# Kernel optimization log

Hardware: AMD Instinct MI355X
Metric: run time of the kernel (lower is better)

Reference implementation:

```python
import jax, jax.numpy as jnp
import numpy as np

D = 512          # sequence_dim
H = 8            # num_heads
DA = 64          # attn_dim per head
DV = 64          # linear_dim per head
NB = 4           # num_blocks
N = 1024         # max_seq_length + max_output_len + 1
B = 4
EPS = 1e-6


def setup_inputs() -> dict:
    key = jax.random.key(0)
    ks = jax.random.split(key, 8)
    sequence = jax.random.normal(ks[0], (B, N, D), dtype=jnp.float32)
    sequence_length = jax.random.randint(ks[1], (B,), 1, 1014)
    pos_embed = jax.random.normal(ks[2], (N, D), dtype=jnp.float32)  # nn.Embedding ~ N(0,1)
    w_uvqk = jax.random.normal(ks[3], (NB, D, 2 * H * DV + 2 * H * DA), dtype=jnp.float32) * 0.02
    w_o = jax.random.normal(ks[4], (NB, H * DV, D), dtype=jnp.float32) * 0.02
    b_o = jnp.zeros((NB, D), dtype=jnp.float32)
    ln1_g = jnp.ones((NB, D), dtype=jnp.float32)
    ln1_b = jnp.zeros((NB, D), dtype=jnp.float32)
    ln2_g = jnp.ones((NB, H * DV), dtype=jnp.float32)
    ln2_b = jnp.zeros((NB, H * DV), dtype=jnp.float32)
    pos_w = jax.random.normal(ks[5], (NB, 2 * N - 1), dtype=jnp.float32) * 0.02
    return {
        'sequence': sequence, 'sequence_length': sequence_length,
        'pos_embed': pos_embed, 'ln1_g': ln1_g, 'ln1_b': ln1_b,
        'w_uvqk': w_uvqk, 'ln2_g': ln2_g, 'ln2_b': ln2_b,
        'w_o': w_o, 'b_o': b_o, 'pos_w': pos_w,
    }


def _layer_norm(x, g, b):
    mu = jnp.mean(x, axis=-1, keepdims=True)
    var = jnp.mean(jnp.square(x - mu), axis=-1, keepdims=True)
    return (x - mu) * jax.lax.rsqrt(var + EPS) * g + b


def reference(sequence, sequence_length, pos_embed, ln1_g, ln1_b, w_uvqk,
              ln2_g, ln2_b, w_o, b_o, pos_w):
    # positional embedding + scale (inference: dropout = identity)
    x = sequence * jnp.asarray(np.sqrt(D), sequence.dtype) + pos_embed[None, :, :]
    # length mask (dense-padded equivalent of the jagged representation)
    mask = (jnp.arange(N)[None, :] < sequence_length[:, None]).astype(sequence.dtype)[..., None]
    x = x * mask
    # invalid_attn_mask = 1 - triu(ones, diag=1): causal incl. diagonal
    causal = jnp.tril(jnp.ones((N, N), sequence.dtype))
    # rel_pos_bias[i, j] = pos_w[j - i + N - 1]
    idx = jnp.arange(N)
    rel = idx[None, :] - idx[:, None] + (N - 1)  # (N, N) in [0, 2N-2]
    for l in range(NB):
        nx = _layer_norm(x, ln1_g[l], ln1_b[l])
        uvqk = jax.nn.silu(nx @ w_uvqk[l])  # (B, N, 2*H*DV + 2*H*DA)
        u, v, q, k = jnp.split(uvqk, [H * DV, 2 * H * DV, 2 * H * DV + H * DA], axis=-1)
        qh = q.reshape(x.shape[0], N, H, DA)
        kh = k.reshape(x.shape[0], N, H, DA)
        vh = v.reshape(x.shape[0], N, H, DV)
        qk = jnp.einsum('bnhd,bmhd->bhnm', qh, kh) + pos_w[l][rel][None, None]
        attn = jax.nn.silu(qk) * (causal / N)  # (B, H, N, N)
        av = jnp.einsum('bhnm,bmhd->bnhd', attn, vh).reshape(x.shape[0], N, H * DV)
        o_in = _layer_norm(av, ln2_g[l], ln2_b[l]) * u
        x = (x + o_in @ w_o[l] + b_o[l]) * mask  # mask = dense<->jagged roundtrip
    # output_embeddings[..., :D] then L2-normalize with clamped norm
    norm = jnp.linalg.norm(x, axis=-1, keepdims=True)
    return x / jnp.clip(norm, 1e-6, None)
```

## Files before the change

### kernel.cpp

```cpp
#include <hip/hip_runtime.h>
#include <math.h>
#include <stdint.h>

#define NN 1024
#define ROWS 4096
#define NBL 4

typedef _Float16 h8 __attribute__((ext_vector_type(8)));
typedef _Float16 h4 __attribute__((ext_vector_type(4)));
typedef float f4 __attribute__((ext_vector_type(4)));

__device__ __forceinline__ float fast_silu(float x) {
    float e = __builtin_amdgcn_exp2f(-1.4426950408889634f * x);
    return x * __builtin_amdgcn_rcpf(1.0f + e);
}

__device__ __forceinline__ void gl16(const void* gp, void* lp) {
    __builtin_amdgcn_global_load_lds(
        (const __attribute__((address_space(1))) uint32_t*)gp,
        (__attribute__((address_space(3))) uint32_t*)lp, 16, 0, 0);
}

__device__ __forceinline__ float wred(float s) {
    #pragma unroll
    for (int off = 1; off < 64; off <<= 1) s += __shfl_xor(s, off);
    return s;
}

__global__ __launch_bounds__(256) void k_transpose16(const float* __restrict__ wuvqk,
                                                     _Float16* __restrict__ wuT,
                                                     const float* __restrict__ wo,
                                                     _Float16* __restrict__ woT) {
    __shared__ _Float16 T[64][66];
    int z = blockIdx.z;
    const float* s; _Float16* d; int N;
    if (z < 4) { N = 2048; s = wuvqk + (size_t)z * 512 * 2048; d = wuT + (size_t)z * 2048 * 512; }
    else {
        if (blockIdx.x >= 8) return;
        N = 512; s = wo + (size_t)(z - 4) * 512 * 512; d = woT + (size_t)(z - 4) * 512 * 512;
    }
    int n0 = blockIdx.x << 6, k0 = blockIdx.y << 6;
    int tx = threadIdx.x & 63, ty = threadIdx.x >> 6;
    #pragma unroll
    for (int q = 0; q < 16; ++q)
        T[(q << 2) + ty][tx] = (_Float16)s[(size_t)(k0 + (q << 2) + ty) * N + n0 + tx];
    __syncthreads();
    #pragma unroll
    for (int q = 0; q < 16; ++q)
        d[(size_t)(n0 + (q << 2) + ty) * 512 + k0 + tx] = T[tx][(q << 2) + ty];
}

template<int MODE>
__global__ __launch_bounds__(256) void k_lnw(const float* __restrict__ X,
                                             const float* __restrict__ X2,
                                             const float* __restrict__ X3,
                                             const float* __restrict__ seq,
                                             const float* __restrict__ pos,
                                             const int* __restrict__ slen,
                                             const float* __restrict__ g,
                                             const float* __restrict__ bt,
                                             _Float16* __restrict__ O,
                                             const _Float16* __restrict__ U,
                                             float* __restrict__ Xw) {
    int tid = threadIdx.x;
    int w = tid >> 6, lane = tid & 63;
    int c = lane << 3;
    #pragma unroll
    for (int rr = 0; rr < 2; ++rr) {
        int row = (blockIdx.x << 3) + (w << 1) + rr;
        float v[8];
        if (MODE == 1) {
            int b = row >> 10, n = row & (NN - 1);
            float m = (n < slen[b]) ? 1.0f : 0.0f;
            const float4* sp = (const float4*)&seq[(size_t)row * 512 + c];
            const float4* pp = (const float4*)&pos[(size_t)n * 512 + c];
            const float SD = 22.627416997969522f;
            float4 s0 = sp[0], s1 = sp[1], p0 = pp[0], p1 = pp[1];
            v[0]=(s0.x*SD+p0.x)*m; v[1]=(s0.y*SD+p0.y)*m; v[2]=(s0.z*SD+p0.z)*m; v[3]=(s0.w*SD+p0.w)*m;
            v[4]=(s1.x*SD+p1.x)*m; v[5]=(s1.y*SD+p1.y)*m; v[6]=(s1.z*SD+p1.z)*m; v[7]=(s1.w*SD+p1.w)*m;
            float4 o0, o1;
            o0.x=v[0]; o0.y=v[1]; o0.z=v[2]; o0.w=v[3];
            o1.x=v[4]; o1.y=v[5]; o1.z=v[6]; o1.w=v[7];
            float4* xp = (float4*)&Xw[(size_t)row * 512 + c];
            xp[0] = o0; xp[1] = o1;
        } else {
            const float4* xp = (const float4*)&X[(size_t)row * 512 + c];
            float4 a = xp[0], b4 = xp[1];
            v[0]=a.x; v[1]=a.y; v[2]=a.z; v[3]=a.w; v[4]=b4.x; v[5]=b4.y; v[6]=b4.z; v[7]=b4.w;
            if (MODE == 2) {
                int nn = row & (NN - 1);
                if (nn >= 384) {
                    const float4* qp = (const float4*)&X2[(size_t)row * 512 + c];
                    float4 t0 = qp[0], t1 = qp[1];
                    v[0]+=t0.x; v[1]+=t0.y; v[2]+=t0.z; v[3]+=t0.w;
                    v[4]+=t1.x; v[5]+=t1.y; v[6]+=t1.z; v[7]+=t1.w;
                }
                if (nn >= 768) {
                    const float4* qp = (const float4*)&X3[(size_t)row * 512 + c];
                    float4 t0 = qp[0], t1 = qp[1];
                    v[0]+=t0.x; v[1]+=t0.y; v[2]+=t0.z; v[3]+=t0.w;
                    v[4]+=t1.x; v[5]+=t1.y; v[6]+=t1.z; v[7]+=t1.w;
                }
            }
        }
        float s = v[0]+v[1]+v[2]+v[3]+v[4]+v[5]+v[6]+v[7];
        s = wred(s);
        float mu = s * (1.0f / 512.0f);
        float ss = 0.0f;
        #pragma unroll
        for (int i = 0; i < 8; ++i) { float d = v[i] - mu; ss += d * d; }
        ss = wred(ss);
        float rs = rsqrtf(ss * (1.0f / 512.0f) + 1e-6f);

        const float4* gp = (const float4*)&g[c];
        const float4* bp = (const float4*)&bt[c];
        float4 g0 = gp[0], g1 = gp[1], b0 = bp[0], b1 = bp[1];
        float gg[8] = {g0.x,g0.y,g0.z,g0.w,g1.x,g1.y,g1.z,g1.w};
        float bb[8] = {b0.x,b0.y,b0.z,b0.w,b1.x,b1.y,b1.z,b1.w};
        float o[8];
        #pragma unroll
        for (int i = 0; i < 8; ++i) o[i] = (v[i] - mu) * rs * gg[i] + bb[i];
        if (MODE == 2) {
            h8 uu = *(const h8*)&U[(size_t)row * 2048 + c];
            #pragma unroll
            for (int i = 0; i < 8; ++i) o[i] *= (float)uu[i];
        }
        h8 oh;
        #pragma unroll
        for (int i = 0; i < 8; ++i) oh[i] = (_Float16)o[i];
        *(h8*)&O[(size_t)row * 512 + c] = oh;
    }
}

__global__ __launch_bounds__(256) void k_normw(float* __restrict__ X) {
    int tid = threadIdx.x;
    int w = tid >> 6, lane = tid & 63;
    int c = lane << 3;
    #pragma unroll
    for (int rr = 0; rr < 2; ++rr) {
        int row = (blockIdx.x << 3) + (w << 1) + rr;
        float4* xp = (float4*)&X[(size_t)row * 512 + c];
        float4 a = xp[0], b4 = xp[1];
        float ss = a.x*a.x + a.y*a.y + a.z*a.z + a.w*a.w +
                   b4.x*b4.x + b4.y*b4.y + b4.z*b4.z + b4.w*b4.w;
        ss = wred(ss);
        float sc = 1.0f / fmaxf(sqrtf(ss), 1e-6f);
        a.x*=sc; a.y*=sc; a.z*=sc; a.w*=sc; b4.x*=sc; b4.y*=sc; b4.z*=sc; b4.w*=sc;
        xp[0] = a; xp[1] = b4;
    }
}

template<int EPI, int BM, int BN, int WAVES, int WGR, int WGC>
__global__ __launch_bounds__(WAVES * 64) void k_gemm(const _Float16* __restrict__ A,
                                                     const _Float16* __restrict__ Bm,
                                                     _Float16* __restrict__ Cu,
                                                     _Float16* __restrict__ vT,
                                                     const float* __restrict__ bo,
                                                     const int* __restrict__ slen,
                                                     float* __restrict__ Xio) {
    constexpr int WR = BM / WGR / 16;
    constexpr int WC = BN / WGC / 16;
    constexpr int QA = BM * 8 / (WAVES * 64);
    constexpr int QB = BN * 8 / (WAVES * 64);
    __shared__ _Float16 smem[2 * 64 * (BM + BN)];
    _Float16* AsB = smem;
    _Float16* BsB = smem + 2 * BM * 64;
    int tid = threadIdx.x;
    int w = tid >> 6, lane = tid & 63;
    int t = lane & 15, gq = lane >> 4;
    int flat = blockIdx.y * gridDim.x + blockIdx.x;
    int cpx = (gridDim.x * gridDim.y) >> 3;
    int f2 = (flat & 7) * cpx + (flat >> 3);
    int bx = f2 % gridDim.x, by = f2 / gridDim.x;
    int row0 = by * BM, col0 = bx * BN;
    int wr = (w / WGC) * (BM / WGR), wc = (w % WGC) * (BN / WGC);

    f4 zero4 = {0.0f, 0.0f, 0.0f, 0.0f};
    f4 acc[WR][WC];
    #pragma unroll
    for (int i = 0; i < WR; ++i)
        #pragma unroll
        for (int j = 0; j < WC; ++j) acc[i][j] = zero4;

    auto stage = [&](int buf, int k0) {
        _Float16* As = AsB + buf * BM * 64;
        _Float16* Bs = BsB + buf * BN * 64;
        #pragma unroll
        for (int q = 0; q < QA; ++q) {
            int s = (q * WAVES + w) * 64 + lane;
            int r = s >> 3, cs = (s & 7) ^ (r & 7);
            gl16(A + (size_t)(row0 + r) * 512 + k0 + (cs << 3),
                 (char*)As + (size_t)(q * WAVES + w) * 1024);
        }
        #pragma unroll
        for (int q = 0; q < QB; ++q) {
            int s = (q * WAVES + w) * 64 + lane;
            int r = s >> 3, cs = (s & 7) ^ (r & 7);
            gl16(Bm + (size_t)(col0 + r) * 512 + k0 + (cs << 3),
                 (char*)Bs + (size_t)(q * WAVES + w) * 1024);
        }
    };

    stage(0, 0);
    int cur = 0;
    for (int k0 = 0; k0 < 512; k0 += 64) {
        __syncthreads();
        if (k0 + 64 < 512) stage(cur ^ 1, k0 + 64);
        const char* As = (const char*)(AsB + cur * BM * 64);
        const char* Bs = (const char*)(BsB + cur * BN * 64);
        h8 af[WR][2], bf[WC][2];
        #pragma unroll
        for (int i = 0; i < WR; ++i) {
            int rl = wr + (i << 4) + t;
            #pragma unroll
            for (int ks = 0; ks < 2; ++ks)
                af[i][ks] = *(const h8*)(As + rl * 128 + (((gq + (ks << 2)) ^ (rl & 7)) << 4));
        }
        #pragma unroll
        for (int j = 0; j < WC; ++j) {
            int nl = wc + (j << 4) + t;
            #pragma unroll
            for (int ks = 0; ks < 2; ++ks)
                bf[j][ks] = *(const h8*)(Bs + nl * 128 + (((gq + (ks << 2)) ^ (nl & 7)) << 4));
        }
        #pragma unroll
        for (int i = 0; i < WR; ++i)
            #pragma unroll
            for (int j = 0; j < WC; ++j) {
                acc[i][j] = __builtin_amdgcn_mfma_f32_16x16x32_f16(af[i][0], bf[j][0], acc[i][j], 0, 0, 0);
                acc[i][j] = __builtin_amdgcn_mfma_f32_16x16x32_f16(af[i][1], bf[j][1], acc[i][j], 0, 0, 0);
            }
        cur ^= 1;
    }

    if (EPI == 0) {
        _Float16* E = smem;
        bool vblk = (col0 >= 512 && col0 < 1024);
        __syncthreads();
        if (vblk) {
            #pragma unroll
            for (int i = 0; i < WR; ++i)
                #pragma unroll
                for (int j = 0; j < WC; ++j) {
                    int cl = wc + (j << 4) + t;
                    int rl = wr + (i << 4) + (gq << 2);
                    h4 pk;
                    #pragma unroll
                    for (int rr = 0; rr < 4; ++rr) pk[rr] = (_Float16)fast_silu(acc[i][j][rr]);
                    *(h4*)&E[cl * 136 + rl] = pk;
                }
        } else {
            #pragma unroll
            for (int i = 0; i < WR; ++i)
                #pragma unroll
                for (int j = 0; j < WC; ++j) {
                    int cl = wc + (j << 4) + t;
                    int rl = wr + (i << 4) + (gq << 2);
                    #pragma unroll
                    for (int rr = 0; rr < 4; ++rr)
                        E[(rl + rr) * 136 + cl] = (_Float16)fast_silu(acc[i][j][rr]);
                }
        }
        __syncthreads();
        constexpr int ITERS = 128 * 16 / (WAVES * 64);
        if (vblk) {
            int b = row0 >> 10;
            int n0l = row0 & 1023;
            #pragma unroll
            for (int it = 0; it < ITERS; ++it) {
                int dl = it * (WAVES * 4) + (tid >> 4);
                int cc = tid & 15;
                h8 vv = *(const h8*)&E[dl * 136 + (cc << 3)];
                int hh = (col0 + dl - 512) >> 6, dd = (col0 + dl - 512) & 63;
                *(h8*)&vT[((size_t)((b << 3) + hh) * 64 + dd) * 1024 + n0l + (cc << 3)] = vv;
            }
        } else {
            #pragma unroll
            for (int it = 0; it < ITERS; ++it) {
                int rl = it * (WAVES * 4) + (tid >> 4);
                int cc = tid & 15;
                h8 vv = *(const h8*)&E[rl * 136 + (cc << 3)];
                *(h8*)&Cu[(size_t)(row0 + rl) * 2048 + col0 + (cc << 3)] = vv;
            }
        }
    } else {
        #pragma unroll
        for (int i = 0; i < WR; ++i) {
            #pragma unroll
            for (int j = 0; j < WC; ++j) {
                int colf = col0 + wc + (j << 4) + t;
                int rowb = row0 + wr + (i << 4) + (gq << 2);
                int b = rowb >> 10;
                #pragma unroll
                for (int rr = 0; rr < 4; ++rr) {
                    int row = rowb + rr;
                    float m = ((row & 1023) < slen[b]) ? 1.0f : 0.0f;
                    size_t ix = (size_t)row * 512 + colf;
                    Xio[ix] = (Xio[ix] + acc[i][j][rr] + bo[colf]) * m;
                }
            }
        }
    }
}

__global__ __launch_bounds__(256) void k_attn(const _Float16* __restrict__ uvqk,
                                              const _Float16* __restrict__ vT,
                                              const float* __restrict__ posw,
                                              float* __restrict__ av0,
                                              float* __restrict__ av1,
                                              float* __restrict__ av2) {
    __shared__ _Float16 Ks[2][64 * 64];
    __shared__ _Float16 Vs[64 * 64];
    __shared__ _Float16 Ps[64 * 72];
    __shared__ float pws[2][128];
    int tid = threadIdx.x;
    int w = tid >> 6, lane = tid & 63;
    int t = lane & 15, gq = lane >> 4;
    int flat = blockIdx.x + 30 * (blockIdx.y + 8 * blockIdx.z);
    int f2 = (flat & 7) * 120 + (flat >> 3);
    int u = f2 % 30, h = (f2 / 30) & 7, b = f2 / 240;

    int nt, mlo, mhi;
    float* avout;
    if (u < 6) { nt = u; mlo = 0; mhi = nt; avout = av0; }
    else if (u < 18) {
        int p = u - 6; nt = 6 + (p >> 1);
        int c0 = (nt + 2) >> 1;
        if (p & 1) { mlo = c0; mhi = nt; avout = av1; }
        else       { mlo = 0;  mhi = c0 - 1; avout = av0; }
    } else {
        int p = u - 18; int third = p / 3; nt = 12 + third; int q3 = p - 3 * third;
        int c = nt + 1, c1 = (c + 2) / 3, c2 = (2 * c + 2) / 3;
        if (q3 == 0)      { mlo = 0;  mhi = c1 - 1; avout = av0; }
        else if (q3 == 1) { mlo = c1; mhi = c2 - 1; avout = av1; }
        else              { mlo = c2; mhi = nt;     avout = av2; }
    }
    int n0 = nt << 6;

    const _Float16* qbase = uvqk + (size_t)b * NN * 2048 + 1024 + h * 64;
    const _Float16* kbase = uvqk + (size_t)b * NN * 2048 + 1536 + h * 64;
    const _Float16* vbase = vT + (size_t)((b << 3) + h) * 64 * 1024;

    #pragma unroll
    for (int q = 0; q < 2; ++q) {
        int s = (((w << 1) + q) << 6) + lane;
        int r = s >> 3, cs = (s & 7) ^ (r & 7);
        gl16(qbase + (size_t)(n0 + r) * 2048 + (cs << 3),
             (char*)&Ks[1][0] + (size_t)(((w << 1) + q) << 6) * 16);
        gl16(kbase + (size_t)((mlo << 6) + r) * 2048 + (cs << 3),
             (char*)&Ks[0][0] + (size_t)(((w << 1) + q) << 6) * 16);
    }
    if (tid < 128) pws[0][tid] = posw[(mlo << 6) - n0 + tid + 960];
    __syncthreads();

    h8 aq[2];
    {
        int rl = (w << 4) + t;
        #pragma unroll
        for (int ks = 0; ks < 2; ++ks)
            aq[ks] = *(const h8*)((const char*)&Ks[1][0] + rl * 128 +
                                  (((gq + (ks << 2)) ^ (rl & 7)) << 4));
    }
    asm volatile("s_waitcnt lgkmcnt(0)" ::: "memory");
    __builtin_amdgcn_sched_barrier(0);
    __syncthreads();

    f4 zero4 = {0.0f, 0.0f, 0.0f, 0.0f};
    f4 avacc[4];
    #pragma unroll
    for (int j = 0; j < 4; ++j) avacc[j] = zero4;

    int cur = 0;
    for (int mt = mlo; mt <= mhi; ++mt) {
        int m0 = mt << 6;
        #pragma unroll
        for (int q = 0; q < 2; ++q) {
            int s = (((w << 1) + q) << 6) + lane;
            int r = s >> 3, cs = (s & 7) ^ (r & 7);
            gl16(vbase + (size_t)r * 1024 + m0 + (cs << 3),
                 (char*)&Vs[0] + (size_t)(((w << 1) + q) << 6) * 16);
        }
        int mt2 = (mt < mhi) ? mt + 1 : mt;
        #pragma unroll
        for (int q = 0; q < 2; ++q) {
            int s = (((w << 1) + q) << 6) + lane;
            int r = s >> 3, cs = (s & 7) ^ (r & 7);
            gl16(kbase + (size_t)((mt2 << 6) + r) * 2048 + (cs << 3),
                 (char*)&Ks[cur ^ 1][0] + (size_t)(((w << 1) + q) << 6) * 16);
        }
        if (tid < 128) pws[cur ^ 1][tid] = posw[(mt2 << 6) - n0 + tid + 960];

        f4 sacc[4];
        __builtin_amdgcn_s_setprio(1);
        #pragma unroll
        for (int i = 0; i < 4; ++i) {
            f4 binit;
            #pragma unroll
            for (int rr = 0; rr < 4; ++rr)
                binit[rr] = pws[cur][63 + (i << 4) + (gq << 2) + rr - ((w << 4) + t)];
            int ml = (i << 4) + t;
            h8 ak0 = *(const h8*)((const char*)&Ks[cur][0] + ml * 128 + (((gq + 0) ^ (ml & 7)) << 4));
            h8 ak1 = *(const h8*)((const char*)&Ks[cur][0] + ml * 128 + (((gq + 4) ^ (ml & 7)) << 4));
            sacc[i] = __builtin_amdgcn_mfma_f32_16x16x32_f16(ak0, aq[0], binit, 0, 0, 0);
            sacc[i] = __builtin_amdgcn_mfma_f32_16x16x32_f16(ak1, aq[1], sacc[i], 0, 0, 0);
        }
        __builtin_amdgcn_s_setprio(0);
        int nabs = n0 + (w << 4) + t;
        #pragma unroll
        for (int i = 0; i < 4; ++i) {
            int mb = m0 + (i << 4) + (gq << 2);
            h4 pk;
            #pragma unroll
            for (int rr = 0; rr < 4; ++rr) {
                float p = (mb + rr <= nabs) ? fast_silu(sacc[i][rr]) : 0.0f;
                pk[rr] = (_Float16)p;
            }
            *(h4*)((char*)Ps + ((w << 4) + t) * 144 + (i << 5) + (gq << 3)) = pk;
        }
        asm volatile("s_waitcnt lgkmcnt(0)" ::: "memory");
        asm volatile("s_waitcnt vmcnt(2)" ::: "memory");
        __builtin_amdgcn_s_barrier();
        __builtin_amdgcn_s_setprio(1);
        #pragma unroll
        for (int ks = 0; ks < 2; ++ks) {
            h8 pa = *(const h8*)((const char*)Ps + ((w << 4) + t) * 144 + (ks << 6) + (gq << 4));
            #pragma unroll
            for (int jt = 0; jt < 4; ++jt) {
                int dl = (jt << 4) + t;
                h8 bv = *(const h8*)((const char*)&Vs[0] + dl * 128 +
                                     (((gq + (ks << 2)) ^ (dl & 7)) << 4));
                avacc[jt] = __builtin_amdgcn_mfma_f32_16x16x32_f16(pa, bv, avacc[jt], 0, 0, 0);
            }
        }
        __builtin_amdgcn_s_setprio(0);
        __syncthreads();
        cur ^= 1;
    }

    #pragma unroll
    for (int jt = 0; jt < 4; ++jt) {
        #pragma unroll
        for (int rr = 0; rr < 4; ++rr) {
            int n = n0 + (w << 4) + (gq << 2) + rr;
            int d = (jt << 4) + t;
            avout[(size_t)(b * NN + n) * 512 + h * 64 + d] = avacc[jt][rr] * (1.0f / 1024.0f);
        }
    }
}

extern "C" void kernel_launch(void* const* d_in, const int* in_sizes, int n_in,
                              void* d_out, int out_size, void* d_ws, size_t ws_size,
                              hipStream_t stream) {
    const float* seq   = (const float*)d_in[0];
    const int*   slen  = (const int*)d_in[1];
    const float* pos   = (const float*)d_in[2];
    const float* ln1g  = (const float*)d_in[3];
    const float* ln1b  = (const float*)d_in[4];
    const float* wuvqk = (const float*)d_in[5];
    const float* ln2g  = (const float*)d_in[6];
    const float* ln2b  = (const float*)d_in[7];
    const float* wo    = (const float*)d_in[8];
    const float* bo    = (const float*)d_in[9];
    const float* posw  = (const float*)d_in[10];

    float* x = (float*)d_out;
    char* W = (char*)d_ws;
    _Float16* nx16   = (_Float16*)(W);
    _Float16* oin16  = (_Float16*)(W + (4u << 20));
    _Float16* uvqk16 = (_Float16*)(W + (8u << 20));
    _Float16* vT16   = (_Float16*)(W + (24u << 20));
    float*    av0    = (float*)   (W + (28u << 20));
    float*    av1    = (float*)   (W + (36u << 20));
    float*    av2    = (float*)   (W + (44u << 20));
    _Float16* wuT16  = (_Float16*)(W + (52u << 20));
    _Float16* woT16  = (_Float16*)(W + (60u << 20));

    k_transpose16<<<dim3(32, 8, 8), 256, 0, stream>>>(wuvqk, wuT16, wo, woT16);
    for (int l = 0; l < NBL; ++l) {
        if (l == 0)
            k_lnw<1><<<512, 256, 0, stream>>>(nullptr, nullptr, nullptr, seq, pos, slen,
                                              ln1g, ln1b, nx16, nullptr, x);
        else
            k_lnw<0><<<512, 256, 0, stream>>>(x, nullptr, nullptr, nullptr, nullptr, nullptr,
                                              ln1g + l * 512, ln1b + l * 512, nx16, nullptr, nullptr);
        k_gemm<0, 128, 128, 8, 2, 4><<<dim3(16, 32), 512, 0, stream>>>(
            nx16, wuT16 + (size_t)l * 2048 * 512, uvqk16, vT16, nullptr, nullptr, nullptr);
        k_attn<<<dim3(30, 8, NBL), 256, 0, stream>>>(uvqk16, vT16, posw + l * (2 * NN - 1),
                                                     av0, av1, av2);
        k_lnw<2><<<512, 256, 0, stream>>>(av0, av1, av2, nullptr, nullptr, nullptr,
                                          ln2g + l * 512, ln2b + l * 512, oin16, uvqk16, nullptr);
        k_gemm<1, 64, 32, 4, 2, 2><<<dim3(16, 64), 256, 0, stream>>>(
            oin16, woT16 + (size_t)l * 512 * 512, nullptr, nullptr, bo + l * 512, slen, x);
    }
    k_normw<<<512, 256, 0, stream>>>(x);
}
```

Baseline: 208.7 us.

## Fuse all layer stages into one cooperative persistent megakernel with grid syncs

Replaces the sequence of about 22 kernel launches with a single cooperative kernel of 512 blocks that loops over transpose, layernorm, GEMM, attention and norm stages, separated by grid-wide syncs. Attention work units are taken from an atomic work queue in a fixed heavy-first order, so the causal load imbalance is spread across blocks. The uvqk GEMM now uses 4 waves instead of 8 per tile. The aim is to remove launch overhead and inter-kernel gaps, at the cost of grid.sync latency, a 64 KB static shared allocation that limits occupancy to 2 blocks per CU, and less efficient GEMM tiling. The old multi-launch path is kept as a fallback when cooperative launch is unavailable.

```diff
diff --git a/kernel.cpp b/kernel.cpp
--- a/kernel.cpp
+++ b/kernel.cpp
@@ -1,6 +1,9 @@
 #include <hip/hip_runtime.h>
+#include <hip/hip_cooperative_groups.h>
 #include <math.h>
 #include <stdint.h>
+
+namespace cg = cooperative_groups;
 
 #define NN 1024
 #define ROWS 4096
@@ -27,20 +30,25 @@
     return s;
 }
 
-__global__ __launch_bounds__(256) void k_transpose16(const float* __restrict__ wuvqk,
-                                                     _Float16* __restrict__ wuT,
-                                                     const float* __restrict__ wo,
-                                                     _Float16* __restrict__ woT) {
-    __shared__ _Float16 T[64][66];
-    int z = blockIdx.z;
-    const float* s; _Float16* d; int N;
-    if (z < 4) { N = 2048; s = wuvqk + (size_t)z * 512 * 2048; d = wuT + (size_t)z * 2048 * 512; }
-    else {
-        if (blockIdx.x >= 8) return;
-        N = 512; s = wo + (size_t)(z - 4) * 512 * 512; d = woT + (size_t)(z - 4) * 512 * 512;
-    }
-    int n0 = blockIdx.x << 6, k0 = blockIdx.y << 6;
-    int tx = threadIdx.x & 63, ty = threadIdx.x >> 6;
+__constant__ int c_order[30] = {5,14,16,17,27, 4,10,12,13,15,18,21,22,24,25,26,28,29,
+                                3,6,8,9,11,19,20,23, 2,7, 1, 0};
+
+__device__ void transpose_unit(int u, char* smem,
+                               const float* __restrict__ wuvqk, _Float16* __restrict__ wuT,
+                               const float* __restrict__ wo, _Float16* __restrict__ woT) {
+    _Float16 (*T)[66] = (_Float16 (*)[66])smem;
+    const float* s; _Float16* d; int N, n0, k0;
+    if (u < 1024) {
+        int z = u >> 8, t = u & 255;
+        N = 2048; s = wuvqk + (size_t)z * 512 * 2048; d = wuT + (size_t)z * 2048 * 512;
+        n0 = (t & 31) << 6; k0 = (t >> 5) << 6;
+    } else {
+        int r2 = u - 1024; int z = r2 >> 6, t = r2 & 63;
+        N = 512; s = wo + (size_t)z * 512 * 512; d = woT + (size_t)z * 512 * 512;
+        n0 = (t & 7) << 6; k0 = (t >> 3) << 6;
+    }
+    int tid = threadIdx.x, tx = tid & 63, ty = tid >> 6;
+    __syncthreads();
     #pragma unroll
     for (int q = 0; q < 16; ++q)
         T[(q << 2) + ty][tx] = (_Float16)s[(size_t)(k0 + (q << 2) + ty) * N + n0 + tx];
@@ -51,23 +59,19 @@
 }
 
 template<int MODE>
-__global__ __launch_bounds__(256) void k_lnw(const float* __restrict__ X,
-                                             const float* __restrict__ X2,
-                                             const float* __restrict__ X3,
-                                             const float* __restrict__ seq,
-                                             const float* __restrict__ pos,
-                                             const int* __restrict__ slen,
-                                             const float* __restrict__ g,
-                                             const float* __restrict__ bt,
-                                             _Float16* __restrict__ O,
-                                             const _Float16* __restrict__ U,
-                                             float* __restrict__ Xw) {
+__device__ void ln_unit(int vb,
+                        const float* __restrict__ X, const float* __restrict__ X2,
+                        const float* __restrict__ X3, const float* __restrict__ seq,
+                        const float* __restrict__ pos, const int* __restrict__ slen,
+                        const float* __restrict__ g, const float* __restrict__ bt,
+                        _Float16* __restrict__ O, const _Float16* __restrict__ U,
+                        float* __restrict__ Xw) {
     int tid = threadIdx.x;
     int w = tid >> 6, lane = tid & 63;
     int c = lane << 3;
     #pragma unroll
     for (int rr = 0; rr < 2; ++rr) {
-        int row = (blockIdx.x << 3) + (w << 1) + rr;
+        int row = (vb << 3) + (w << 1) + rr;
         float v[8];
         if (MODE == 1) {
             int b = row >> 10, n = row & (NN - 1);
@@ -132,13 +136,13 @@
     }
 }
 
-__global__ __launch_bounds__(256) void k_normw(float* __restrict__ X) {
+__device__ void norm_unit(int vb, float* __restrict__ X) {
     int tid = threadIdx.x;
     int w = tid >> 6, lane = tid & 63;
     int c = lane << 3;
     #pragma unroll
     for (int rr = 0; rr < 2; ++rr) {
-        int row = (blockIdx.x << 3) + (w << 1) + rr;
+        int row = (vb << 3) + (w << 1) + rr;
         float4* xp = (float4*)&X[(size_t)row * 512 + c];
         float4 a = xp[0], b4 = xp[1];
         float ss = a.x*a.x + a.y*a.y + a.z*a.z + a.w*a.w +
@@ -151,29 +155,27 @@
 }
 
 template<int EPI, int BM, int BN, int WAVES, int WGR, int WGC>
-__global__ __launch_bounds__(WAVES * 64) void k_gemm(const _Float16* __restrict__ A,
-                                                     const _Float16* __restrict__ Bm,
-                                                     _Float16* __restrict__ Cu,
-                                                     _Float16* __restrict__ vT,
-                                                     const float* __restrict__ bo,
-                                                     const int* __restrict__ slen,
-                                                     float* __restrict__ Xio) {
+__device__ void gemm_unit(int unit, int nbx, int nunits, char* smemc,
+                          const _Float16* __restrict__ A, const _Float16* __restrict__ Bm,
+                          _Float16* __restrict__ Cu, _Float16* __restrict__ vT,
+                          const float* __restrict__ bo, const int* __restrict__ slen,
+                          float* __restrict__ Xio) {
     constexpr int WR = BM / WGR / 16;
     constexpr int WC = BN / WGC / 16;
     constexpr int QA = BM * 8 / (WAVES * 64);
     constexpr int QB = BN * 8 / (WAVES * 64);
-    __shared__ _Float16 smem[2 * 64 * (BM + BN)];
-    _Float16* AsB = smem;
-    _Float16* BsB = smem + 2 * BM * 64;
+    _Float16* AsB = (_Float16*)smemc;
+    _Float16* BsB = (_Float16*)smemc + 2 * BM * 64;
     int tid = threadIdx.x;
     int w = tid >> 6, lane = tid & 63;
     int t = lane & 15, gq = lane >> 4;
-    int flat = blockIdx.y * gridDim.x + blockIdx.x;
-    int cpx = (gridDim.x * gridDim.y) >> 3;
-    int f2 = (flat & 7) * cpx + (flat >> 3);
-    int bx = f2 % gridDim.x, by = f2 / gridDim.x;
+    int cpx = nunits >> 3;
+    int f2 = (unit & 7) * cpx + (unit >> 3);
+    int bx = f2 % nbx, by = f2 / nbx;
     int row0 = by * BM, col0 = bx * BN;
     int wr = (w / WGC) * (BM / WGR), wc = (w % WGC) * (BN / WGC);
+
+    __syncthreads();
 
     f4 zero4 = {0.0f, 0.0f, 0.0f, 0.0f};
     f4 acc[WR][WC];
@@ -234,7 +236,7 @@
     }
 
     if (EPI == 0) {
-        _Float16* E = smem;
+        _Float16* E = (_Float16*)smemc;
         bool vblk = (col0 >= 512 && col0 < 1024);
         __syncthreads();
         if (vblk) {
@@ -303,25 +305,20 @@
     }
 }
 
-__global__ __launch_bounds__(256) void k_attn(const _Float16* __restrict__ uvqk,
-                                              const _Float16* __restrict__ vT,
-                                              const float* __restrict__ posw,
-                                              float* __restrict__ av0,
-                                              float* __restrict__ av1,
-                                              float* __restrict__ av2) {
-    __shared__ _Float16 Ks[2][64 * 64];
-    __shared__ _Float16 Vs[64 * 64];
-    __shared__ _Float16 Ps[64 * 72];
-    __shared__ float pws[2][128];
+__device__ void attn_unit(int b, int h, int u, char* smem,
+                          const _Float16* __restrict__ uvqk, const _Float16* __restrict__ vTg,
+                          const float* __restrict__ pw,
+                          float* __restrict__ av0, float* __restrict__ av1,
+                          float* __restrict__ av2) {
     int tid = threadIdx.x;
     int w = tid >> 6, lane = tid & 63;
     int t = lane & 15, gq = lane >> 4;
-    int flat = blockIdx.x + 30 * (blockIdx.y + 8 * blockIdx.z);
-    int f2 = (flat & 7) * 120 + (flat >> 3);
-    int u = f2 % 30, h = (f2 / 30) & 7, b = f2 / 240;
-
-    int nt, mlo, mhi;
-    float* avout;
+    char* KsBase = smem;
+    char* VsBase = smem + 16384;
+    char* Ps     = smem + 24576;
+    float* pws   = (float*)(smem + 33792);
+
+    int nt, mlo, mhi; float* avout;
     if (u < 6) { nt = u; mlo = 0; mhi = nt; avout = av0; }
     else if (u < 18) {
         int p = u - 6; nt = 6 + (p >> 1);
@@ -339,18 +336,16 @@
 
     const _Float16* qbase = uvqk + (size_t)b * NN * 2048 + 1024 + h * 64;
     const _Float16* kbase = uvqk + (size_t)b * NN * 2048 + 1536 + h * 64;
-    const _Float16* vbase = vT + (size_t)((b << 3) + h) * 64 * 1024;
+    const _Float16* vbase = vTg + (size_t)((b << 3) + h) * 64 * 1024;
 
     #pragma unroll
     for (int q = 0; q < 2; ++q) {
         int s = (((w << 1) + q) << 6) + lane;
         int r = s >> 3, cs = (s & 7) ^ (r & 7);
-        gl16(qbase + (size_t)(n0 + r) * 2048 + (cs << 3),
-             (char*)&Ks[1][0] + (size_t)(((w << 1) + q) << 6) * 16);
-        gl16(kbase + (size_t)((mlo << 6) + r) * 2048 + (cs << 3),
-             (char*)&Ks[0][0] + (size_t)(((w << 1) + q) << 6) * 16);
-    }
-    if (tid < 128) pws[0][tid] = posw[(mlo << 6) - n0 + tid + 960];
+        gl16(qbase + (size_t)(n0 + r) * 2048 + (cs << 3), KsBase + 8192 + (((w << 1) + q) << 10));
+        gl16(kbase + (size_t)((mlo << 6) + r) * 2048 + (cs << 3), KsBase + (((w << 1) + q) << 10));
+    }
+    if (tid < 128) pws[tid] = pw[(mlo << 6) - n0 + tid + 960];
     __syncthreads();
 
     h8 aq[2];
@@ -358,8 +353,7 @@
         int rl = (w << 4) + t;
         #pragma unroll
         for (int ks = 0; ks < 2; ++ks)
-            aq[ks] = *(const h8*)((const char*)&Ks[1][0] + rl * 128 +
-                                  (((gq + (ks << 2)) ^ (rl & 7)) << 4));
+            aq[ks] = *(const h8*)(KsBase + 8192 + rl * 128 + (((gq + (ks << 2)) ^ (rl & 7)) << 4));
     }
     asm volatile("s_waitcnt lgkmcnt(0)" ::: "memory");
     __builtin_amdgcn_sched_barrier(0);
@@ -377,8 +371,7 @@
         for (int q = 0; q < 2; ++q) {
             int s = (((w << 1) + q) << 6) + lane;
             int r = s >> 3, cs = (s & 7) ^ (r & 7);
-            gl16(vbase + (size_t)r * 1024 + m0 + (cs << 3),
-                 (char*)&Vs[0] + (size_t)(((w << 1) + q) << 6) * 16);
+            gl16(vbase + (size_t)r * 1024 + m0 + (cs << 3), VsBase + (((w << 1) + q) << 10));
         }
         int mt2 = (mt < mhi) ? mt + 1 : mt;
         #pragma unroll
@@ -386,10 +379,11 @@
             int s = (((w << 1) + q) << 6) + lane;
             int r = s >> 3, cs = (s & 7) ^ (r & 7);
             gl16(kbase + (size_t)((mt2 << 6) + r) * 2048 + (cs << 3),
-                 (char*)&Ks[cur ^ 1][0] + (size_t)(((w << 1) + q) << 6) * 16);
-        }
-        if (tid < 128) pws[cur ^ 1][tid] = posw[(mt2 << 6) - n0 + tid + 960];
-
+                 KsBase + ((cur ^ 1) << 13) + (((w << 1) + q) << 10));
+        }
+        if (tid < 128) pws[((cur ^ 1) << 7) + tid] = pw[(mt2 << 6) - n0 + tid + 960];
+
+        const char* Kc = KsBase + (cur << 13);
         f4 sacc[4];
         __builtin_amdgcn_s_setprio(1);
         #pragma unroll
@@ -397,10 +391,10 @@
             f4 binit;
             #pragma unroll
             for (int rr = 0; rr < 4; ++rr)
-                binit[rr] = pws[cur][63 + (i << 4) + (gq << 2) + rr - ((w << 4) + t)];
+                binit[rr] = pws[(cur << 7) + 63 + (i << 4) + (gq << 2) + rr - ((w << 4) + t)];
             int ml = (i << 4) + t;
-            h8 ak0 = *(const h8*)((const char*)&Ks[cur][0] + ml * 128 + (((gq + 0) ^ (ml & 7)) << 4));
-            h8 ak1 = *(const h8*)((const char*)&Ks[cur][0] + ml * 128 + (((gq + 4) ^ (ml & 7)) << 4));
+            h8 ak0 = *(const h8*)(Kc + ml * 128 + (((gq + 0) ^ (ml & 7)) << 4));
+            h8 ak1 = *(const h8*)(Kc + ml * 128 + (((gq + 4) ^ (ml & 7)) << 4));
             sacc[i] = __builtin_amdgcn_mfma_f32_16x16x32_f16(ak0, aq[0], binit, 0, 0, 0);
             sacc[i] = __builtin_amdgcn_mfma_f32_16x16x32_f16(ak1, aq[1], sacc[i], 0, 0, 0);
         }
@@ -415,7 +409,7 @@
                 float p = (mb + rr <= nabs) ? fast_silu(sacc[i][rr]) : 0.0f;
                 pk[rr] = (_Float16)p;
             }
-            *(h4*)((char*)Ps + ((w << 4) + t) * 144 + (i << 5) + (gq << 3)) = pk;
+            *(h4*)(Ps + ((w << 4) + t) * 144 + (i << 5) + (gq << 3)) = pk;
         }
         asm volatile("s_waitcnt lgkmcnt(0)" ::: "memory");
         asm volatile("s_waitcnt vmcnt(2)" ::: "memory");
@@ -423,12 +417,11 @@
         __builtin_amdgcn_s_setprio(1);
         #pragma unroll
         for (int ks = 0; ks < 2; ++ks) {
-            h8 pa = *(const h8*)((const char*)Ps + ((w << 4) + t) * 144 + (ks << 6) + (gq << 4));
+            h8 pa = *(const h8*)(Ps + ((w << 4) + t) * 144 + (ks << 6) + (gq << 4));
             #pragma unroll
             for (int jt = 0; jt < 4; ++jt) {
                 int dl = (jt << 4) + t;
-                h8 bv = *(const h8*)((const char*)&Vs[0] + dl * 128 +
-                                     (((gq + (ks << 2)) ^ (dl & 7)) << 4));
+                h8 bv = *(const h8*)(VsBase + dl * 128 + (((gq + (ks << 2)) ^ (dl & 7)) << 4));
                 avacc[jt] = __builtin_amdgcn_mfma_f32_16x16x32_f16(pa, bv, avacc[jt], 0, 0, 0);
             }
         }
@@ -448,49 +441,163 @@
     }
 }
 
+__global__ __launch_bounds__(256) void k_transpose16(const float* wuvqk, _Float16* wuT,
+                                                     const float* wo, _Float16* woT) {
+    __shared__ __align__(16) char smem[8448];
+    transpose_unit(blockIdx.x, smem, wuvqk, wuT, wo, woT);
+}
+
+template<int MODE>
+__global__ __launch_bounds__(256) void k_lnw(const float* X, const float* X2, const float* X3,
+                                             const float* seq, const float* pos, const int* slen,
+                                             const float* g, const float* bt,
+                                             _Float16* O, const _Float16* U, float* Xw) {
+    ln_unit<MODE>(blockIdx.x, X, X2, X3, seq, pos, slen, g, bt, O, U, Xw);
+}
+
+__global__ __launch_bounds__(256) void k_normw(float* X) { norm_unit(blockIdx.x, X); }
+
+template<int EPI, int BM, int BN, int WAVES, int WGR, int WGC>
+__global__ __launch_bounds__(WAVES * 64) void k_gemm(const _Float16* A, const _Float16* Bm,
+                                                     _Float16* Cu, _Float16* vT,
+                                                     const float* bo, const int* slen, float* Xio) {
+    __shared__ __align__(16) char smem[(BM + BN) * 256];
+    gemm_unit<EPI, BM, BN, WAVES, WGR, WGC>(blockIdx.y * gridDim.x + blockIdx.x, gridDim.x,
+                                            gridDim.x * gridDim.y, smem, A, Bm, Cu, vT, bo, slen, Xio);
+}
+
+__global__ __launch_bounds__(256) void k_attn(const _Float16* uvqk, const _Float16* vT,
+                                              const float* posw, float* av0, float* av1, float* av2) {
+    __shared__ __align__(16) char smem[34816];
+    int flat = blockIdx.x + 30 * (blockIdx.y + 8 * blockIdx.z);
+    int f2 = (flat & 7) * 120 + (flat >> 3);
+    int u = f2 % 30, h = (f2 / 30) & 7, b = f2 / 240;
+    attn_unit(b, h, u, smem, uvqk, vT, posw, av0, av1, av2);
+}
+
+struct MegaArgs {
+    const float *seq, *pos, *ln1g, *ln1b, *ln2g, *ln2b, *wuvqk, *wo, *bo, *posw;
+    const int* slen;
+    float *x, *av0, *av1, *av2;
+    _Float16 *nx, *oin, *uvqk, *vT, *wuT, *woT;
+    unsigned int* ctr;
+};
+
+__global__ __launch_bounds__(256, 2) void k_mega(MegaArgs P) {
+    cg::grid_group grid = cg::this_grid();
+    __shared__ __align__(16) char smem[65536];
+    int tid = threadIdx.x, bid = blockIdx.x, G = gridDim.x;
+
+    if (bid == 0 && tid < 4) atomicExch(&P.ctr[tid], 0u);
+    for (int u = bid; u < 1280; u += G)
+        transpose_unit(u, smem, P.wuvqk, P.wuT, P.wo, P.woT);
+    for (int vb = bid; vb < 512; vb += G)
+        ln_unit<1>(vb, nullptr, nullptr, nullptr, P.seq, P.pos, P.slen, P.ln1g, P.ln1b,
+                   P.nx, nullptr, P.x);
+    grid.sync();
+
+    for (int l = 0; l < NBL; ++l) {
+        if (l > 0) {
+            for (int vb = bid; vb < 512; vb += G)
+                ln_unit<0>(vb, P.x, nullptr, nullptr, nullptr, nullptr, nullptr,
+                           P.ln1g + l * 512, P.ln1b + l * 512, P.nx, nullptr, nullptr);
+            grid.sync();
+        }
+        for (int u = bid; u < 512; u += G)
+            gemm_unit<0, 128, 128, 4, 2, 2>(u, 16, 512, smem, P.nx,
+                                            P.wuT + (size_t)l * 2048 * 512,
+                                            P.uvqk, P.vT, nullptr, nullptr, nullptr);
+        grid.sync();
+        {
+            volatile int* sm_u = (volatile int*)(smem + 35840);
+            const float* pw = P.posw + l * 2047;
+            for (;;) {
+                __syncthreads();
+                if (tid == 0) *sm_u = (int)atomicAdd(&P.ctr[l], 1u);
+                __syncthreads();
+                int p = *sm_u;
+                if (p >= 960) break;
+                int bh = p & 31;
+                attn_unit(bh >> 3, bh & 7, c_order[p >> 5], smem, P.uvqk, P.vT, pw,
+                          P.av0, P.av1, P.av2);
+            }
+        }
+        grid.sync();
+        for (int vb = bid; vb < 512; vb += G)
+            ln_unit<2>(vb, P.av0, P.av1, P.av2, nullptr, nullptr, nullptr,
+                       P.ln2g + l * 512, P.ln2b + l * 512, P.oin, P.uvqk, nullptr);
+        grid.sync();
+        for (int u = bid; u < 1024; u += G)
+            gemm_unit<1, 64, 32, 4, 2, 2>(u, 16, 1024, smem, P.oin,
+                                          P.woT + (size_t)l * 512 * 512,
+                                          nullptr, nullptr, P.bo + l * 512, P.slen, P.x);
+        grid.sync();
+    }
+    for (int vb = bid; vb < 512; vb += G)
+        norm_unit(vb, P.x);
+}
+
 extern "C" void kernel_launch(void* const* d_in, const int* in_sizes, int n_in,
                               void* d_out, int out_size, void* d_ws, size_t ws_size,
                               hipStream_t stream) {
-    const float* seq   = (const float*)d_in[0];
-    const int*   slen  = (const int*)d_in[1];
-    const float* pos   = (const float*)d_in[2];
-    const float* ln1g  = (const float*)d_in[3];
-    const float* ln1b  = (const float*)d_in[4];
-    const float* wuvqk = (const float*)d_in[5];
-    const float* ln2g  = (const float*)d_in[6];
-    const float* ln2b  = (const float*)d_in[7];
-    const float* wo    = (const float*)d_in[8];
-    const float* bo    = (const float*)d_in[9];
-    const float* posw  = (const float*)d_in[10];
-
-    float* x = (float*)d_out;
     char* W = (char*)d_ws;
-    _Float16* nx16   = (_Float16*)(W);
-    _Float16* oin16  = (_Float16*)(W + (4u << 20));
-    _Float16* uvqk16 = (_Float16*)(W + (8u << 20));
-    _Float16* vT16   = (_Float16*)(W + (24u << 20));
-    float*    av0    = (float*)   (W + (28u << 20));
-    float*    av1    = (float*)   (W + (36u << 20));
-    float*    av2    = (float*)   (W + (44u << 20));
-    _Float16* wuT16  = (_Float16*)(W + (52u << 20));
-    _Float16* woT16  = (_Float16*)(W + (60u << 20));
-
-    k_transpose16<<<dim3(32, 8, 8), 256, 0, stream>>>(wuvqk, wuT16, wo, woT16);
-    for (int l = 0; l < NBL; ++l) {
-        if (l == 0)
-            k_lnw<1><<<512, 256, 0, stream>>>(nullptr, nullptr, nullptr, seq, pos, slen,
-                                              ln1g, ln1b, nx16, nullptr, x);
-        else
-            k_lnw<0><<<512, 256, 0, stream>>>(x, nullptr, nullptr, nullptr, nullptr, nullptr,
-                                              ln1g + l * 512, ln1b + l * 512, nx16, nullptr, nullptr);
-        k_gemm<0, 128, 128, 8, 2, 4><<<dim3(16, 32), 512, 0, stream>>>(
-            nx16, wuT16 + (size_t)l * 2048 * 512, uvqk16, vT16, nullptr, nullptr, nullptr);
-        k_attn<<<dim3(30, 8, NBL), 256, 0, stream>>>(uvqk16, vT16, posw + l * (2 * NN - 1),
-                                                     av0, av1, av2);
-        k_lnw<2><<<512, 256, 0, stream>>>(av0, av1, av2, nullptr, nullptr, nullptr,
-                                          ln2g + l * 512, ln2b + l * 512, oin16, uvqk16, nullptr);
-        k_gemm<1, 64, 32, 4, 2, 2><<<dim3(16, 64), 256, 0, stream>>>(
-            oin16, woT16 + (size_t)l * 512 * 512, nullptr, nullptr, bo + l * 512, slen, x);
-    }
-    k_normw<<<512, 256, 0, stream>>>(x);
-}
+    MegaArgs P;
+    P.seq   = (const float*)d_in[0];
+    P.slen  = (const int*)d_in[1];
+    P.pos   = (const float*)d_in[2];
+    P.ln1g  = (const float*)d_in[3];
+    P.ln1b  = (const float*)d_in[4];
+    P.wuvqk = (const float*)d_in[5];
+    P.ln2g  = (const float*)d_in[6];
+    P.ln2b  = (const float*)d_in[7];
+    P.wo    = (const float*)d_in[8];
+    P.bo    = (const float*)d_in[9];
+    P.posw  = (const float*)d_in[10];
+    P.x    = (float*)d_out;
+    P.nx   = (_Float16*)(W);
+    P.oin  = (_Float16*)(W + (4u << 20));
+    P.uvqk = (_Float16*)(W + (8u << 20));
+    P.vT   = (_Float16*)(W + (24u << 20));
+    P.av0  = (float*)   (W + (28u << 20));
+    P.av1  = (float*)   (W + (36u << 20));
+    P.av2  = (float*)   (W + (44u << 20));
+    P.wuT  = (_Float16*)(W + (52u << 20));
+    P.woT  = (_Float16*)(W + (60u << 20));
+    P.ctr  = (unsigned int*)(W + (62u << 20));
+
+    bool done = false;
+    int coopAttr = 0;
+    if (hipDeviceGetAttribute(&coopAttr, hipDeviceAttributeCooperativeLaunch, 0) == hipSuccess &&
+        coopAttr != 0) {
+        int maxB = 0;
+        if (hipOccupancyMaxActiveBlocksPerMultiprocessor(&maxB, (const void*)k_mega, 256, 0) ==
+                hipSuccess && maxB >= 2) {
+            void* kp[] = { &P };
+            done = (hipLaunchCooperativeKernel((const void*)k_mega, dim3(512), dim3(256),
+                                               kp, 0, stream) == hipSuccess);
+        }
+    }
+    if (!done) {
+        k_transpose16<<<1280, 256, 0, stream>>>(P.wuvqk, P.wuT, P.wo, P.woT);
+        for (int l = 0; l < NBL; ++l) {
+            if (l == 0)
+                k_lnw<1><<<512, 256, 0, stream>>>(nullptr, nullptr, nullptr, P.seq, P.pos, P.slen,
+                                                  P.ln1g, P.ln1b, P.nx, nullptr, P.x);
+            else
+                k_lnw<0><<<512, 256, 0, stream>>>(P.x, nullptr, nullptr, nullptr, nullptr, nullptr,
+                                                  P.ln1g + l * 512, P.ln1b + l * 512, P.nx,
+                                                  nullptr, nullptr);
+            k_gemm<0, 128, 128, 8, 2, 4><<<dim3(16, 32), 512, 0, stream>>>(
+                P.nx, P.wuT + (size_t)l * 2048 * 512, P.uvqk, P.vT, nullptr, nullptr, nullptr);
+            k_attn<<<dim3(30, 8, NBL), 256, 0, stream>>>(P.uvqk, P.vT, P.posw + l * 2047,
+                                                         P.av0, P.av1, P.av2);
+            k_lnw<2><<<512, 256, 0, stream>>>(P.av0, P.av1, P.av2, nullptr, nullptr, nullptr,
+                                              P.ln2g + l * 512, P.ln2b + l * 512, P.oin,
+                                              P.uvqk, nullptr);
+            k_gemm<1, 64, 32, 4, 2, 2><<<dim3(16, 64), 256, 0, stream>>>(
+                P.oin, P.woT + (size_t)l * 512 * 512, nullptr, nullptr, P.bo + l * 512,
+                P.slen, P.x);
+        }
+        k_normw<<<512, 256, 0, stream>>>(P.x);
+    }
+}
```

Measured after the change: 209.0 us. About the same (+0.1%).
